# Kernel tuning notes

Hardware: AMD Instinct MI355X
Metric: run time of the kernel (lower is better)

Reference implementation:

```python
import jax, jax.numpy as jnp
import numpy as np

B, N, C = 4, 2048, 1024
H = 16
D = C // H  # head_dim = 64

def setup_inputs() -> dict:
    key = jax.random.key(0)
    k1, k2, k3 = jax.random.split(key, 3)
    s = 1.0 / np.sqrt(C)
    x = jax.random.normal(k1, (B, N, C), dtype=jnp.float32)
    qkv_w = jax.random.normal(k2, (3 * C, C), dtype=jnp.float32) * s
    proj_w = jax.random.normal(k3, (C, C), dtype=jnp.float32) * s
    proj_b = jnp.zeros((C,), dtype=jnp.float32)
    return {"x": x, "qkv_w": qkv_w, "proj_w": proj_w, "proj_b": proj_b}

def reference(x, qkv_w, proj_w, proj_b):
    # qkv: torch Linear -> x @ W^T, no bias
    qkv = jnp.einsum('bnc,oc->bno', x, qkv_w)            # [B,N,3C]
    qkv = qkv.reshape(B, N, 3, H, D)
    q, k, v = qkv[:, :, 0], qkv[:, :, 1], qkv[:, :, 2]   # [B,N,H,D]
    scale = D ** -0.5
    scores = jnp.einsum('bqhd,bkhd->bhqk', q, k) * scale  # [B,H,N,N]
    causal = jnp.tril(jnp.ones((N, N), dtype=bool))
    scores = jnp.where(causal[None, None], scores, -jnp.inf)
    attn = jax.nn.softmax(scores, axis=-1)
    out = jnp.einsum('bhqk,bkhd->bqhd', attn, v).reshape(B, N, C)
    out = jnp.einsum('bnc,oc->bno', out, proj_w) + proj_b
    return out
```

## Files before the change

### kernel.cpp

```cpp
#include <hip/hip_runtime.h>
#include <math.h>

typedef __attribute__((ext_vector_type(8))) short short8;
typedef __attribute__((ext_vector_type(4))) short short4v;
typedef __attribute__((ext_vector_type(4))) float f32x4;
typedef __attribute__((ext_vector_type(4))) _Float16 half4v;

#define B_  4
#define N_  2048
#define C_  1024
#define H_  16
#define D_  64
#define TC3 3072

__device__ __forceinline__ short f2bf(float f) {
    unsigned u = __builtin_bit_cast(unsigned, f);
    u += 0x7fffu + ((u >> 16) & 1u);
    return (short)(u >> 16);
}

__device__ __forceinline__ half4v pack4h(float a, float b, float cc, float d) {
    auto lo = __builtin_amdgcn_cvt_pkrtz(a, b);
    auto hi = __builtin_amdgcn_cvt_pkrtz(cc, d);
    auto v4 = __builtin_shufflevector(lo, hi, 0, 1, 2, 3);
    return __builtin_bit_cast(half4v, v4);
}

__device__ __forceinline__ void gload16(const void* g, void* l) {
    __builtin_amdgcn_global_load_lds(
        (const __attribute__((address_space(1))) void*)g,
        (__attribute__((address_space(3))) void*)l, 16, 0, 0);
}

#define NX8  (B_ * N_ * C_ / 8)
#define NQ8  (TC3 * C_ / 8)
#define NP8  (C_ * C_ / 8)

__global__ __launch_bounds__(256) void cast_all(const float* __restrict__ x,
                                                const float* __restrict__ wq,
                                                const float* __restrict__ wp,
                                                short* __restrict__ xb,
                                                short* __restrict__ wqb,
                                                short* __restrict__ wpb) {
    int i = blockIdx.x * 256 + threadIdx.x;
    const float* src;
    short* dst;
    if (i < NX8) { src = x; dst = xb; }
    else if (i < NX8 + NQ8) { i -= NX8; src = wq; dst = wqb; }
    else { i -= NX8 + NQ8; src = wp; dst = wpb; }
    const float4 a = ((const float4*)src)[2 * i];
    const float4 b = ((const float4*)src)[2 * i + 1];
    short8 t;
    t[0] = f2bf(a.x); t[1] = f2bf(a.y); t[2] = f2bf(a.z); t[3] = f2bf(a.w);
    t[4] = f2bf(b.x); t[5] = f2bf(b.y); t[6] = f2bf(b.z); t[7] = f2bf(b.w);
    ((short8*)dst)[i] = t;
}

#define GK 64

template <int MODE>
__global__ __launch_bounds__(256) void gemm_bf16(const short* __restrict__ A,
                                                 const short* __restrict__ Bw,
                                                 const float* __restrict__ bias,
                                                 short* __restrict__ Qb,
                                                 short* __restrict__ Kb,
                                                 _Float16* __restrict__ Vtb,
                                                 float* __restrict__ Fout,
                                                 int M, int Nn, int K) {
    __shared__ short smem[2 * 128 * GK];
    short* As = smem;
    short* Bs = smem + 128 * GK;

    const int tid = threadIdx.x;
    const int w = tid >> 6;
    const int ln = tid & 63;
    const int wm = w >> 1;
    const int wn = w & 1;
    const int c = ln & 15;
    const int g = ln >> 4;
    const int c7 = c & 7;

    const int m0 = blockIdx.y * 128;
    const int n0 = blockIdx.x * 128;

    f32x4 acc[4][4];
#pragma unroll
    for (int m = 0; m < 4; ++m)
#pragma unroll
        for (int n = 0; n < 4; ++n) acc[m][n] = (f32x4){0.f, 0.f, 0.f, 0.f};

    const int srow = ln >> 3;
    const int sseg = (ln & 7) ^ srow;

    for (int k0 = 0; k0 < K; k0 += GK) {
#pragma unroll
        for (int j = 0; j < 4; ++j) {
            const int R0 = w * 32 + j * 8;
            const int row = R0 + srow;
            gload16(A + (size_t)(m0 + row) * K + k0 + sseg * 8, &As[R0 * GK]);
            gload16(Bw + (size_t)(n0 + row) * K + k0 + sseg * 8, &Bs[R0 * GK]);
        }
        asm volatile("s_waitcnt vmcnt(0)" ::: "memory");
        __syncthreads();

#pragma unroll
        for (int kh = 0; kh < 2; ++kh) {
            short8 aF[4], bF[4];
#pragma unroll
            for (int m = 0; m < 4; ++m)
                aF[m] = *(const short8*)&As[(wm * 64 + m * 16 + c) * GK +
                                            (((kh * 4 + g) ^ c7) * 8)];
#pragma unroll
            for (int n = 0; n < 4; ++n)
                bF[n] = *(const short8*)&Bs[(wn * 64 + n * 16 + c) * GK +
                                            (((kh * 4 + g) ^ c7) * 8)];
#pragma unroll
            for (int m = 0; m < 4; ++m)
#pragma unroll
                for (int n = 0; n < 4; ++n)
                    acc[m][n] = __builtin_amdgcn_mfma_f32_16x16x32_bf16(aF[m], bF[n], acc[m][n], 0, 0, 0);
        }
        __syncthreads();
    }

    if (MODE == 0) {
        const int mat = n0 >> 10;
        if (mat == 2) {
#pragma unroll
            for (int m = 0; m < 4; ++m) {
                const int row = m0 + wm * 64 + m * 16 + g * 4;
                const int b = row >> 11;
                const int nseq = row & 2047;
#pragma unroll
                for (int n = 0; n < 4; ++n) {
                    const int col = n0 + wn * 64 + n * 16 + c;
                    const int h = (col >> 6) & 15;
                    const int d = col & 63;
                    const half4v p = pack4h(acc[m][n][0], acc[m][n][1],
                                            acc[m][n][2], acc[m][n][3]);
                    *(half4v*)&Vtb[((size_t)(b * 16 + h) * 64 + d) * N_ + nseq] = p;
                }
            }
        } else {
            short* base = (mat == 0) ? Qb : Kb;
#pragma unroll
            for (int p = 0; p < 2; ++p) {
                __syncthreads();
                if (wn == p) {
#pragma unroll
                    for (int m = 0; m < 4; ++m)
#pragma unroll
                        for (int n = 0; n < 4; ++n)
#pragma unroll
                            for (int r = 0; r < 4; ++r)
                                smem[(wm * 64 + m * 16 + g * 4 + r) * 64 +
                                     (((n ^ g) * 16) + c)] = f2bf(acc[m][n][r]);
                }
                __syncthreads();
                const int row = tid >> 1;
                const int col0 = (tid & 1) * 32;
                const int gg = (row >> 2) & 3;
                const int grow = m0 + row;
                const int bb = grow >> 11, nseq = grow & 2047;
                const int h = ((n0 + p * 64) >> 6) & 15;
                short* dst = base + ((size_t)(bb * 16 + h) * N_ + nseq) * D_ + col0;
#pragma unroll
                for (int s16 = 0; s16 < 2; ++s16) {
                    const int Cb = col0 + s16 * 16;
                    const int ls_off = row * 64 + ((((Cb >> 4) ^ gg)) << 4);
                    *(short8*)(dst + s16 * 16) = *(const short8*)&smem[ls_off];
                    *(short8*)(dst + s16 * 16 + 8) = *(const short8*)&smem[ls_off + 8];
                }
            }
        }
    } else {
#pragma unroll
        for (int m = 0; m < 4; ++m) {
            const int row = m0 + wm * 64 + m * 16 + g * 4;
#pragma unroll
            for (int n = 0; n < 4; ++n) {
                const int col = n0 + wn * 64 + n * 16 + c;
                const float bv = bias[col];
#pragma unroll
                for (int r = 0; r < 4; ++r)
                    Fout[(size_t)(row + r) * Nn + col] = acc[m][n][r] + bv;
            }
        }
    }
}


__device__ __forceinline__ void stage_kv(const short* __restrict__ gK,
                                         const short* __restrict__ gV,
                                         short* KsB, short* VsB,
                                         int kt, int w, int lane) {
    const int sub = lane >> 3;
    const int sseg = (lane & 7) ^ sub;
#pragma unroll
    for (int j = 0; j < 2; ++j) {
        const int R0 = w * 16 + j * 8;
        const int row = R0 + sub;
        gload16(gK + (size_t)(kt * 64 + row) * D_ + sseg * 8, KsB + R0 * 64);
        gload16(gV + (size_t)row * N_ + kt * 64 + sseg * 8, VsB + R0 * 64);
    }
}

__global__ __launch_bounds__(256, 4) void attn_fused(const short* __restrict__ Qb,
                                                     const short* __restrict__ Kb,
                                                     const _Float16* __restrict__ Vtb,
                                                     short* __restrict__ attnb) {
    __shared__ short Ks[2][64 * 64];
    __shared__ short Vts[2][64 * 64];

    const int tid = threadIdx.x;
    const int w = tid >> 6;
    const int lane = tid & 63;
    const int g = lane >> 4;
    const int c = lane & 15;
    const int swz = c & 7;

    const int bh = blockIdx.x >> 4;
    const int p = blockIdx.x & 15;
    const int b = bh >> 4, h = bh & 15;

    const int uu[2] = {p, 31 - p};
    const int rb[2] = {p * 64 + w * 16, (31 - p) * 64 + w * 16};
    const int nkt = uu[1] + 1;

    const short* gK = Kb + (size_t)bh * N_ * D_;
    const short* gV = (const short*)(Vtb + (size_t)bh * D_ * N_);

    short8 aQ[2][2];
#pragma unroll
    for (int m = 0; m < 2; ++m) {
        const short* qb0 = Qb + ((size_t)bh * N_ + rb[m]) * D_;
        aQ[m][0] = *(const short8*)(qb0 + c * D_ + g * 8);
        aQ[m][1] = *(const short8*)(qb0 + c * D_ + 32 + g * 8);
    }

    f32x4 Oacc[2][4];
#pragma unroll
    for (int m = 0; m < 2; ++m)
#pragma unroll
        for (int nt = 0; nt < 4; ++nt) Oacc[m][nt] = (f32x4){0.f, 0.f, 0.f, 0.f};
    float ls[2] = {0.f, 0.f};

    stage_kv(gK, gV, Ks[0], Vts[0], 0, w, lane);

    for (int kt = 0; kt < nkt; ++kt) {
        const short* KsB = Ks[kt & 1];
        const short* VsB = Vts[kt & 1];
        asm volatile("s_waitcnt vmcnt(0)" ::: "memory");
        __syncthreads();
        if (kt + 1 < nkt)
            stage_kv(gK, gV, Ks[(kt + 1) & 1], Vts[(kt + 1) & 1], kt + 1, w, lane);

        const int kvb = kt * 64;

        f32x4 S[2][4];
        __builtin_amdgcn_s_setprio(1);
#pragma unroll
        for (int n = 0; n < 4; ++n) {
            const bool a1 = (kvb + n * 16 <= rb[1] + 15);
            const bool a0 = (kvb + n * 16 <= rb[0] + 15);
            if (!a1) continue;
            const short* kr = KsB + (n * 16 + c) * 64;
            const short8 bk0 = *(const short8*)(kr + (g ^ swz) * 8);
            const short8 bk1 = *(const short8*)(kr + ((4 + g) ^ swz) * 8);
            f32x4 s1 = (f32x4){0.f, 0.f, 0.f, 0.f};
            s1 = __builtin_amdgcn_mfma_f32_16x16x32_bf16(bk0, aQ[1][0], s1, 0, 0, 0);
            s1 = __builtin_amdgcn_mfma_f32_16x16x32_bf16(bk1, aQ[1][1], s1, 0, 0, 0);
            S[1][n] = s1;
            if (a0) {
                f32x4 s0 = (f32x4){0.f, 0.f, 0.f, 0.f};
                s0 = __builtin_amdgcn_mfma_f32_16x16x32_bf16(bk0, aQ[0][0], s0, 0, 0, 0);
                s0 = __builtin_amdgcn_mfma_f32_16x16x32_bf16(bk1, aQ[0][1], s0, 0, 0, 0);
                S[0][n] = s0;
            }
        }
        __builtin_amdgcn_s_setprio(0);

        half4v Pb[2][4];
#pragma unroll
        for (int m = 0; m < 2; ++m) {
            const int qrow = rb[m] + c;
            const bool dm = (kt == uu[m]);
#pragma unroll
            for (int n = 0; n < 4; ++n) {
                if (kvb + n * 16 > rb[m] + 15) continue;
                float pv0[4];
#pragma unroll
                for (int r = 0; r < 4; ++r) {
                    float pv = __expf(fmaf(S[m][n][r], 0.125f, -4.0f));
                    if (dm && (kvb + n * 16 + g * 4 + r) > qrow) pv = 0.f;
                    ls[m] += pv;
                    pv0[r] = pv;
                }
                Pb[m][n] = pack4h(pv0[0], pv0[1], pv0[2], pv0[3]);
            }
        }

        __builtin_amdgcn_s_setprio(1);
#pragma unroll
        for (int n = 0; n < 4; ++n) {
            const bool a1 = (kvb + n * 16 <= rb[1] + 15);
            const bool a0 = (kvb + n * 16 <= rb[0] + 15);
            if (!a1) continue;
#pragma unroll
            for (int nt = 0; nt < 4; ++nt) {
                const int vrow = nt * 16 + c;
                const int vseg = (n * 2 + (g >> 1)) ^ swz;
                const half4v av = *(const half4v*)&VsB[vrow * 64 + vseg * 8 + (g & 1) * 4];
                Oacc[1][nt] = __builtin_amdgcn_mfma_f32_16x16x16f16(av, Pb[1][n], Oacc[1][nt], 0, 0, 0);
                if (a0)
                    Oacc[0][nt] = __builtin_amdgcn_mfma_f32_16x16x16f16(av, Pb[0][n], Oacc[0][nt], 0, 0, 0);
            }
        }
        __builtin_amdgcn_s_setprio(0);
    }

#pragma unroll
    for (int m = 0; m < 2; ++m) {
        ls[m] += __shfl_xor(ls[m], 16);
        ls[m] += __shfl_xor(ls[m], 32);
    }
#pragma unroll
    for (int m = 0; m < 2; ++m) {
        const float inv = 1.0f / ls[m];
        const int qrow = rb[m] + c;
        short* dst = attnb + (size_t)(b * N_ + qrow) * C_ + h * D_;
#pragma unroll
        for (int nt = 0; nt < 4; ++nt) {
            short4v o;
#pragma unroll
            for (int r = 0; r < 4; ++r) o[r] = f2bf(Oacc[m][nt][r] * inv);
            *(short4v*)(dst + nt * 16 + g * 4) = o;
        }
    }
}

extern "C" void kernel_launch(void* const* d_in, const int* in_sizes, int n_in,
                              void* d_out, int out_size, void* d_ws, size_t ws_size,
                              hipStream_t stream) {
    const float* x      = (const float*)d_in[0];
    const float* qkv_w  = (const float*)d_in[1];
    const float* proj_w = (const float*)d_in[2];
    const float* proj_b = (const float*)d_in[3];
    float* out = (float*)d_out;

    short* xb      = (short*)d_ws;
    short* qkv_wb  = xb + (size_t)B_ * N_ * C_;
    short* proj_wb = qkv_wb + (size_t)TC3 * C_;
    short* Qb      = proj_wb + (size_t)C_ * C_;
    short* Kb      = Qb + (size_t)B_ * H_ * N_ * D_;
    _Float16* Vtb  = (_Float16*)(Kb + (size_t)B_ * H_ * N_ * D_);
    short* attnb   = (short*)(Vtb + (size_t)B_ * H_ * N_ * D_);

    const int M = B_ * N_;
    dim3 blk(256);

    cast_all<<<dim3((NX8 + NQ8 + NP8) / 256), blk, 0, stream>>>(
        x, qkv_w, proj_w, xb, qkv_wb, proj_wb);

    gemm_bf16<0><<<dim3(TC3 / 128, M / 128), blk, 0, stream>>>(
        xb, qkv_wb, nullptr, Qb, Kb, Vtb, nullptr, M, TC3, C_);

    attn_fused<<<dim3(1024), blk, 0, stream>>>(Qb, Kb, Vtb, attnb);

    gemm_bf16<1><<<dim3(C_ / 128, M / 128), blk, 0, stream>>>(
        attnb, proj_wb, proj_b, nullptr, nullptr, nullptr, out, M, C_, C_);
}
```

Baseline: 296.2 us.

## Double query rows per attention block to reuse staged K/V tiles

Each attention block now handles two 128-row query tiles (paired causally as t and 15-t), with each wave owning 32 rows instead of 16. Every K/V tile staged in shared memory therefore feeds twice as many MFMAs, halving K/V global traffic and staging per query row. The grid is halved to 512 blocks, block IDs are remapped to interleave heads, and launch bounds drop to 2 blocks per SM. The cost is more registers and less occupancy, which can hurt latency hiding.

```diff
diff --git a/kernel.cpp b/kernel.cpp
--- a/kernel.cpp
+++ b/kernel.cpp
@@ -205,7 +205,7 @@
     }
 }
 
-__global__ __launch_bounds__(256, 4) void attn_fused(const short* __restrict__ Qb,
+__global__ __launch_bounds__(256, 2) void attn_fused(const short* __restrict__ Qb,
                                                      const short* __restrict__ Kb,
                                                      const _Float16* __restrict__ Vtb,
                                                      short* __restrict__ attnb) {
@@ -219,31 +219,35 @@
     const int c = lane & 15;
     const int swz = c & 7;
 
-    const int bh = blockIdx.x >> 4;
-    const int p = blockIdx.x & 15;
+    const int item = (blockIdx.x & 7) * 64 + (blockIdx.x >> 3);
+    const int bh = item >> 3;
+    const int t = item & 7;
     const int b = bh >> 4, h = bh & 15;
 
-    const int uu[2] = {p, 31 - p};
-    const int rb[2] = {p * 64 + w * 16, (31 - p) * 64 + w * 16};
-    const int nkt = uu[1] + 1;
+    const int rm[2] = {t * 128 + w * 32, (15 - t) * 128 + w * 32};
+    const int nkt = 32 - 2 * t;
 
     const short* gK = Kb + (size_t)bh * N_ * D_;
     const short* gV = (const short*)(Vtb + (size_t)bh * D_ * N_);
 
-    short8 aQ[2][2];
-#pragma unroll
-    for (int m = 0; m < 2; ++m) {
-        const short* qb0 = Qb + ((size_t)bh * N_ + rb[m]) * D_;
-        aQ[m][0] = *(const short8*)(qb0 + c * D_ + g * 8);
-        aQ[m][1] = *(const short8*)(qb0 + c * D_ + 32 + g * 8);
-    }
-
-    f32x4 Oacc[2][4];
-#pragma unroll
-    for (int m = 0; m < 2; ++m)
-#pragma unroll
-        for (int nt = 0; nt < 4; ++nt) Oacc[m][nt] = (f32x4){0.f, 0.f, 0.f, 0.f};
-    float ls[2] = {0.f, 0.f};
+    short8 aQ[2][2][2];
+#pragma unroll
+    for (int T = 0; T < 2; ++T)
+#pragma unroll
+        for (int m = 0; m < 2; ++m) {
+            const short* q0 = Qb + ((size_t)bh * N_ + rm[T] + m * 16 + c) * D_;
+            aQ[T][m][0] = *(const short8*)(q0 + g * 8);
+            aQ[T][m][1] = *(const short8*)(q0 + 32 + g * 8);
+        }
+
+    f32x4 Oacc[2][2][4];
+#pragma unroll
+    for (int T = 0; T < 2; ++T)
+#pragma unroll
+        for (int m = 0; m < 2; ++m)
+#pragma unroll
+            for (int nt = 0; nt < 4; ++nt) Oacc[T][m][nt] = (f32x4){0.f, 0.f, 0.f, 0.f};
+    float ls[2][2] = {{0.f, 0.f}, {0.f, 0.f}};
 
     stage_kv(gK, gV, Ks[0], Vts[0], 0, w, lane);
 
@@ -257,86 +261,102 @@
 
         const int kvb = kt * 64;
 
-        f32x4 S[2][4];
+        f32x4 S[2][2][4];
         __builtin_amdgcn_s_setprio(1);
 #pragma unroll
         for (int n = 0; n < 4; ++n) {
-            const bool a1 = (kvb + n * 16 <= rb[1] + 15);
-            const bool a0 = (kvb + n * 16 <= rb[0] + 15);
+            const bool a1 = (kvb + n * 16 <= rm[1] + 31);
+            const bool a0 = (kvb + n * 16 <= rm[0] + 31);
             if (!a1) continue;
             const short* kr = KsB + (n * 16 + c) * 64;
             const short8 bk0 = *(const short8*)(kr + (g ^ swz) * 8);
             const short8 bk1 = *(const short8*)(kr + ((4 + g) ^ swz) * 8);
-            f32x4 s1 = (f32x4){0.f, 0.f, 0.f, 0.f};
-            s1 = __builtin_amdgcn_mfma_f32_16x16x32_bf16(bk0, aQ[1][0], s1, 0, 0, 0);
-            s1 = __builtin_amdgcn_mfma_f32_16x16x32_bf16(bk1, aQ[1][1], s1, 0, 0, 0);
-            S[1][n] = s1;
+#pragma unroll
+            for (int m = 0; m < 2; ++m) {
+                f32x4 s1 = (f32x4){0.f, 0.f, 0.f, 0.f};
+                s1 = __builtin_amdgcn_mfma_f32_16x16x32_bf16(bk0, aQ[1][m][0], s1, 0, 0, 0);
+                s1 = __builtin_amdgcn_mfma_f32_16x16x32_bf16(bk1, aQ[1][m][1], s1, 0, 0, 0);
+                S[1][m][n] = s1;
+            }
             if (a0) {
-                f32x4 s0 = (f32x4){0.f, 0.f, 0.f, 0.f};
-                s0 = __builtin_amdgcn_mfma_f32_16x16x32_bf16(bk0, aQ[0][0], s0, 0, 0, 0);
-                s0 = __builtin_amdgcn_mfma_f32_16x16x32_bf16(bk1, aQ[0][1], s0, 0, 0, 0);
-                S[0][n] = s0;
+#pragma unroll
+                for (int m = 0; m < 2; ++m) {
+                    f32x4 s0 = (f32x4){0.f, 0.f, 0.f, 0.f};
+                    s0 = __builtin_amdgcn_mfma_f32_16x16x32_bf16(bk0, aQ[0][m][0], s0, 0, 0, 0);
+                    s0 = __builtin_amdgcn_mfma_f32_16x16x32_bf16(bk1, aQ[0][m][1], s0, 0, 0, 0);
+                    S[0][m][n] = s0;
+                }
             }
         }
         __builtin_amdgcn_s_setprio(0);
 
-        half4v Pb[2][4];
-#pragma unroll
-        for (int m = 0; m < 2; ++m) {
-            const int qrow = rb[m] + c;
-            const bool dm = (kt == uu[m]);
-#pragma unroll
-            for (int n = 0; n < 4; ++n) {
-                if (kvb + n * 16 > rb[m] + 15) continue;
-                float pv0[4];
-#pragma unroll
-                for (int r = 0; r < 4; ++r) {
-                    float pv = __expf(fmaf(S[m][n][r], 0.125f, -4.0f));
-                    if (dm && (kvb + n * 16 + g * 4 + r) > qrow) pv = 0.f;
-                    ls[m] += pv;
-                    pv0[r] = pv;
-                }
-                Pb[m][n] = pack4h(pv0[0], pv0[1], pv0[2], pv0[3]);
+        half4v Pb[2][2][4];
+#pragma unroll
+        for (int T = 0; T < 2; ++T) {
+            const bool needmask = (kvb + 63) > rm[T];
+#pragma unroll
+            for (int m = 0; m < 2; ++m) {
+                const int qrow = rm[T] + m * 16 + c;
+#pragma unroll
+                for (int n = 0; n < 4; ++n) {
+                    if (kvb + n * 16 > rm[T] + 31) continue;
+                    float pv0[4];
+#pragma unroll
+                    for (int r = 0; r < 4; ++r) {
+                        float pv = __expf(fmaf(S[T][m][n][r], 0.125f, -4.0f));
+                        if (needmask && (kvb + n * 16 + g * 4 + r) > qrow) pv = 0.f;
+                        ls[T][m] += pv;
+                        pv0[r] = pv;
+                    }
+                    Pb[T][m][n] = pack4h(pv0[0], pv0[1], pv0[2], pv0[3]);
+                }
             }
         }
 
         __builtin_amdgcn_s_setprio(1);
 #pragma unroll
         for (int n = 0; n < 4; ++n) {
-            const bool a1 = (kvb + n * 16 <= rb[1] + 15);
-            const bool a0 = (kvb + n * 16 <= rb[0] + 15);
+            const bool a1 = (kvb + n * 16 <= rm[1] + 31);
+            const bool a0 = (kvb + n * 16 <= rm[0] + 31);
             if (!a1) continue;
 #pragma unroll
             for (int nt = 0; nt < 4; ++nt) {
                 const int vrow = nt * 16 + c;
                 const int vseg = (n * 2 + (g >> 1)) ^ swz;
                 const half4v av = *(const half4v*)&VsB[vrow * 64 + vseg * 8 + (g & 1) * 4];
-                Oacc[1][nt] = __builtin_amdgcn_mfma_f32_16x16x16f16(av, Pb[1][n], Oacc[1][nt], 0, 0, 0);
-                if (a0)
-                    Oacc[0][nt] = __builtin_amdgcn_mfma_f32_16x16x16f16(av, Pb[0][n], Oacc[0][nt], 0, 0, 0);
+                Oacc[1][0][nt] = __builtin_amdgcn_mfma_f32_16x16x16f16(av, Pb[1][0][n], Oacc[1][0][nt], 0, 0, 0);
+                Oacc[1][1][nt] = __builtin_amdgcn_mfma_f32_16x16x16f16(av, Pb[1][1][n], Oacc[1][1][nt], 0, 0, 0);
+                if (a0) {
+                    Oacc[0][0][nt] = __builtin_amdgcn_mfma_f32_16x16x16f16(av, Pb[0][0][n], Oacc[0][0][nt], 0, 0, 0);
+                    Oacc[0][1][nt] = __builtin_amdgcn_mfma_f32_16x16x16f16(av, Pb[0][1][n], Oacc[0][1][nt], 0, 0, 0);
+                }
             }
         }
         __builtin_amdgcn_s_setprio(0);
     }
 
 #pragma unroll
-    for (int m = 0; m < 2; ++m) {
-        ls[m] += __shfl_xor(ls[m], 16);
-        ls[m] += __shfl_xor(ls[m], 32);
-    }
-#pragma unroll
-    for (int m = 0; m < 2; ++m) {
-        const float inv = 1.0f / ls[m];
-        const int qrow = rb[m] + c;
-        short* dst = attnb + (size_t)(b * N_ + qrow) * C_ + h * D_;
-#pragma unroll
-        for (int nt = 0; nt < 4; ++nt) {
-            short4v o;
-#pragma unroll
-            for (int r = 0; r < 4; ++r) o[r] = f2bf(Oacc[m][nt][r] * inv);
-            *(short4v*)(dst + nt * 16 + g * 4) = o;
-        }
-    }
+    for (int T = 0; T < 2; ++T)
+#pragma unroll
+        for (int m = 0; m < 2; ++m) {
+            ls[T][m] += __shfl_xor(ls[T][m], 16);
+            ls[T][m] += __shfl_xor(ls[T][m], 32);
+        }
+#pragma unroll
+    for (int T = 0; T < 2; ++T)
+#pragma unroll
+        for (int m = 0; m < 2; ++m) {
+            const float inv = 1.0f / ls[T][m];
+            const int qrow = rm[T] + m * 16 + c;
+            short* dst = attnb + (size_t)(b * N_ + qrow) * C_ + h * D_;
+#pragma unroll
+            for (int nt = 0; nt < 4; ++nt) {
+                short4v o;
+#pragma unroll
+                for (int r = 0; r < 4; ++r) o[r] = f2bf(Oacc[T][m][nt][r] * inv);
+                *(short4v*)(dst + nt * 16 + g * 4) = o;
+            }
+        }
 }
 
 extern "C" void kernel_launch(void* const* d_in, const int* in_sizes, int n_in,
@@ -365,7 +385,7 @@
     gemm_bf16<0><<<dim3(TC3 / 128, M / 128), blk, 0, stream>>>(
         xb, qkv_wb, nullptr, Qb, Kb, Vtb, nullptr, M, TC3, C_);
 
-    attn_fused<<<dim3(1024), blk, 0, stream>>>(Qb, Kb, Vtb, attnb);
+    attn_fused<<<dim3(512), blk, 0, stream>>>(Qb, Kb, Vtb, attnb);
 
     gemm_bf16<1><<<dim3(C_ / 128, M / 128), blk, 0, stream>>>(
         attnb, proj_wb, proj_b, nullptr, nullptr, nullptr, out, M, C_, C_);
```

Measured after the change: 285.0 us. -3.8%, faster.
